# Performance work log

Measured on AMD Instinct MI355X. Metric: run time of the kernel, lower is better.

Reference implementation:

```python
import jax, jax.numpy as jnp
import numpy as np
from jax import lax

B, T, H = 4096, 2048, 32


def setup_inputs() -> dict:
    key = jax.random.key(0)
    ks = jax.random.split(key, 10)
    s = 1.0 / np.sqrt(H)  # PyTorch LSTM/Linear init scale
    x = jax.random.normal(ks[0], (B, T, 1), dtype=jnp.float32)
    lengths = jax.random.randint(ks[1], (B,), 1, T + 1, dtype=jnp.int32)
    u = lambda k, shape, sc: jax.random.uniform(k, shape, jnp.float32, -sc, sc)
    return {
        "x": x,
        "lengths": lengths,
        # backward-direction LSTM weights (only h_n[-1] is used by the head)
        "w_ih": u(ks[2], (4 * H, 1), s),
        "w_hh": u(ks[3], (4 * H, H), s),
        "b_ih": u(ks[4], (4 * H,), s),
        "b_hh": u(ks[5], (4 * H,), s),
        "fc_w": u(ks[6], (64, H), 1.0 / np.sqrt(H)),
        "fc_b": u(ks[7], (64,), 1.0 / np.sqrt(H)),
        "fc2_w": u(ks[8], (1, 64), 1.0 / np.sqrt(64)),
        "fc2_b": u(ks[9], (1,), 1.0 / np.sqrt(64)),
    }


def _backward_lstm_final(x, lengths, w_ih, w_hh, b_ih, b_hh):
    """Final hidden state of the backward direction of a packed BiLSTM.

    The backward direction reads each sequence from t=len-1 down to t=0 with
    zero initial state. Equivalently: scan padded x in reverse time order and
    only update (h, c) where t < length (packed-sequence semantics).
    """
    Bv, Tv, _ = x.shape
    ts = jnp.arange(Tv - 1, -1, -1)                       # reversed time indices
    xs_t = jnp.transpose(x[:, ::-1, :], (1, 0, 2))        # [T, B, 1]
    mask_t = ts[:, None] < lengths[None, :]               # [T, B]

    def step(carry, inp):
        h, c = carry
        xt, m = inp                                        # [B,1], [B]
        gates = xt @ w_ih.T + b_ih + h @ w_hh.T + b_hh     # [B, 4H]
        i, f, g, o = jnp.split(gates, 4, axis=-1)
        i = jax.nn.sigmoid(i)
        f = jax.nn.sigmoid(f)
        g = jnp.tanh(g)
        o = jax.nn.sigmoid(o)
        c_new = f * c + i * g
        h_new = o * jnp.tanh(c_new)
        mm = m[:, None]
        return (jnp.where(mm, h_new, h), jnp.where(mm, c_new, c)), None

    h0 = jnp.zeros((Bv, H), dtype=x.dtype)
    c0 = jnp.zeros((Bv, H), dtype=x.dtype)
    (h_n, _), _ = lax.scan(step, (h0, c0), (xs_t, mask_t))
    return h_n                                             # [B, H]


def reference(x, lengths, w_ih, w_hh, b_ih, b_hh, fc_w, fc_b, fc2_w, fc2_b):
    h_n = _backward_lstm_final(x, lengths, w_ih, w_hh, b_ih, b_hh)
    out = jax.nn.elu(h_n @ fc_w.T + fc_b)                  # [B, 64]
    out = jax.nn.sigmoid(out @ fc2_w.T + fc2_b)            # [B, 1]
    return out
```

## Files before the change

kernel.cpp:

```cpp
#include <hip/hip_runtime.h>
#include <hip/hip_bf16.h>

constexpr int BB = 4096;
constexpr int TT = 2048;
constexpr int HH = 32;

typedef float v2f __attribute__((ext_vector_type(2)));
typedef float v4f __attribute__((ext_vector_type(4)));
typedef _Float16 v2h __attribute__((ext_vector_type(2)));
typedef _Float16 v8h __attribute__((ext_vector_type(8)));

__device__ __forceinline__ float fexp2(float x) { return __builtin_amdgcn_exp2f(x); }
__device__ __forceinline__ float frcp(float x)  { return __builtin_amdgcn_rcpf(x); }
__device__ __forceinline__ float fsigmoid(float x) {
    return frcp(1.0f + fexp2(x * -1.4426950408889634f));
}
__device__ __forceinline__ float felu(float x) {
    return x > 0.0f ? x : (fexp2(x * 1.4426950408889634f) - 1.0f);
}

__global__ void sort_by_len_kernel(const int* __restrict__ lengths, int* __restrict__ perm) {
    __shared__ int hist[TT];
    __shared__ int csum[256];
    const int tid = threadIdx.x;
    for (int i = tid; i < TT; i += 256) hist[i] = 0;
    __syncthreads();
    for (int i = tid; i < BB; i += 256) atomicAdd(&hist[TT - lengths[i]], 1);
    __syncthreads();
    const int base = tid * 8;
    int loc[8];
    int s = 0;
#pragma unroll
    for (int j = 0; j < 8; ++j) { loc[j] = hist[base + j]; s += loc[j]; }
    csum[tid] = s;
    __syncthreads();
    for (int off = 1; off < 256; off <<= 1) {
        int v = (tid >= off) ? csum[tid - off] : 0;
        __syncthreads();
        csum[tid] += v;
        __syncthreads();
    }
    int run = csum[tid] - s;
#pragma unroll
    for (int j = 0; j < 8; ++j) { int t = loc[j]; hist[base + j] = run; run += t; }
    __syncthreads();
    for (int i = tid; i < BB; i += 256) {
        int pos = atomicAdd(&hist[TT - lengths[i]], 1);
        perm[pos] = i;
    }
}

__global__ __attribute__((amdgpu_flat_work_group_size(64, 64), amdgpu_waves_per_eu(1, 4)))
void lstm_kernel(const float* __restrict__ x, const int* __restrict__ lengths,
                 const float* __restrict__ w_ih, const float* __restrict__ w_hh,
                 const float* __restrict__ b_ih, const float* __restrict__ b_hh,
                 const float* __restrict__ fc_w, const float* __restrict__ fc_b,
                 const float* __restrict__ fc2_w, const float* __restrict__ fc2_b,
                 float* __restrict__ out, const int* __restrict__ perm) {
    __shared__ __align__(16) _Float16 hs[64];
    __shared__ float xbuf[64];

    const int lane = threadIdx.x;

    const int r0 = lane;
    const int r1 = lane + 64;

    const bool  lower  = lane < 32;
    const float NL2E   = -1.4426950408889634f;
    const float scale0 = NL2E;
    const float scale1 = lower ? 2.0f * NL2E : NL2E;
    const float amul   = lower ? 2.0f : 1.0f;
    const float badd   = lower ? -1.0f : 0.0f;

    v2h w0[16], w1[16];
    {
        const v2f* p0 = reinterpret_cast<const v2f*>(w_hh + r0 * 32);
        const v2f* p1 = reinterpret_cast<const v2f*>(w_hh + r1 * 32);
#pragma unroll
        for (int q = 0; q < 16; ++q) {
            v2f a = p0[q]; v2f bq = p1[q];
            w0[q] = (v2h){(_Float16)(a.x * scale0), (_Float16)(a.y * scale0)};
            w1[q] = (v2h){(_Float16)(bq.x * scale1), (_Float16)(bq.y * scale1)};
        }
    }
    const float wi0 = w_ih[r0] * scale0;
    const float wi1 = w_ih[r1] * scale1;
    const float bi0 = (b_ih[r0] + b_hh[r0]) * scale0;
    const float bi1 = (b_ih[r1] + b_hh[r1]) * scale1;

#pragma unroll
    for (int q = 0; q < 16; ++q) {
        asm volatile("" : "+v"(w0[q]), "+v"(w1[q]));
    }

    for (int phase = 0; phase < 2; ++phase) {
        const int k = phase ? (BB - 1 - (int)blockIdx.x) : (int)blockIdx.x;
        const int b = perm ? perm[k] : k;
        const int L = lengths[b];

        v8h hr[4];
#pragma unroll
        for (int q = 0; q < 4; ++q) hr[q] = (v8h)(_Float16)0.0f;
        float c = 0.0f;
        const float* xb = x + (size_t)b * TT;

        int t = L - 1;
        while (t >= 0) {
            const int tb = t & ~63;
            xbuf[lane] = xb[tb + lane];
            for (; t >= tb; --t) {
                const float xt = xbuf[t - tb];
                float a0  = fmaf(wi0, xt, bi0);
                float a1  = fmaf(wi1, xt, bi1);
                float a0b = 0.0f, a1b = 0.0f;
#pragma unroll
                for (int q = 0; q < 4; ++q) {
                    const v8h hh = hr[q];
                    const v2h p01 = __builtin_shufflevector(hh, hh, 0, 1);
                    const v2h p23 = __builtin_shufflevector(hh, hh, 2, 3);
                    const v2h p45 = __builtin_shufflevector(hh, hh, 4, 5);
                    const v2h p67 = __builtin_shufflevector(hh, hh, 6, 7);
                    a0  = __builtin_amdgcn_fdot2(w0[4*q+0], p01, a0,  false);
                    a0b = __builtin_amdgcn_fdot2(w0[4*q+1], p23, a0b, false);
                    a0  = __builtin_amdgcn_fdot2(w0[4*q+2], p45, a0,  false);
                    a0b = __builtin_amdgcn_fdot2(w0[4*q+3], p67, a0b, false);
                    a1  = __builtin_amdgcn_fdot2(w1[4*q+0], p01, a1,  false);
                    a1b = __builtin_amdgcn_fdot2(w1[4*q+1], p23, a1b, false);
                    a1  = __builtin_amdgcn_fdot2(w1[4*q+2], p45, a1,  false);
                    a1b = __builtin_amdgcn_fdot2(w1[4*q+3], p67, a1b, false);
                }
                const float g0 = a0 + a0b;
                const float g1 = a1 + a1b;
                const float s0 = frcp(1.0f + fexp2(g0));
                const float s1 = frcp(1.0f + fexp2(g1));
                const float v1 = fmaf(amul, s1, badd);
                const float ig = s0 * v1;
                const float igx = __shfl_xor(ig, 32);
                c = fmaf(s0, c, igx);
                const float tc = 1.0f - 2.0f * frcp(1.0f + fexp2(c * 2.8853900817779268f));
                const float hn = v1 * tc;
                hs[lane] = (_Float16)hn;
                const v8h* hp = reinterpret_cast<const v8h*>(hs + 32);
#pragma unroll
                for (int q = 0; q < 4; ++q) hr[q] = hp[q];
            }
        }

        float hf[32];
#pragma unroll
        for (int q = 0; q < 4; ++q) {
            const v8h hh = hr[q];
#pragma unroll
            for (int j = 0; j < 8; ++j) hf[8 * q + j] = (float)hh[j];
        }
        float a = fc_b[lane];
        {
            const v4f* fp = reinterpret_cast<const v4f*>(fc_w + lane * 32);
#pragma unroll
            for (int q = 0; q < 8; ++q) {
                const v4f f = fp[q];
                a = fmaf(f.x, hf[4 * q + 0], a);
                a = fmaf(f.y, hf[4 * q + 1], a);
                a = fmaf(f.z, hf[4 * q + 2], a);
                a = fmaf(f.w, hf[4 * q + 3], a);
            }
        }
        float partial = felu(a) * fc2_w[lane];
#pragma unroll
        for (int m = 32; m >= 1; m >>= 1) partial += __shfl_xor(partial, m, 64);
        if (lane == 0) out[b] = fsigmoid(partial + fc2_b[0]);
    }
}

extern "C" void kernel_launch(void* const* d_in, const int* in_sizes, int n_in,
                              void* d_out, int out_size, void* d_ws, size_t ws_size,
                              hipStream_t stream) {
    const float* x       = (const float*)d_in[0];
    const int*   lengths = (const int*)d_in[1];
    const float* w_ih    = (const float*)d_in[2];
    const float* w_hh    = (const float*)d_in[3];
    const float* b_ih    = (const float*)d_in[4];
    const float* b_hh    = (const float*)d_in[5];
    const float* fc_w    = (const float*)d_in[6];
    const float* fc_b    = (const float*)d_in[7];
    const float* fc2_w   = (const float*)d_in[8];
    const float* fc2_b   = (const float*)d_in[9];
    float* out = (float*)d_out;

    int* perm = nullptr;
    if (ws_size >= (size_t)BB * sizeof(int)) {
        perm = (int*)d_ws;
        hipLaunchKernelGGL(sort_by_len_kernel, dim3(1), dim3(256), 0, stream, lengths, perm);
    }
    hipLaunchKernelGGL(lstm_kernel, dim3(BB / 2), dim3(64), 0, stream,
                       x, lengths, w_ih, w_hh, b_ih, b_hh,
                       fc_w, fc_b, fc2_w, fc2_b, out, perm);
}
```

Before: 675.9 us.

## Broadcast hidden state via DPP and readlane instead of LDS round-trip

The per-step hidden-state exchange no longer goes through shared memory. Each lane packs its fp16 h with its neighbour's via a DPP quad swap, and 16 readlane ops broadcast the packed values from the upper half-wave into scalar registers. The x values come from a register via readlane instead of an LDS buffer, and the next 64-element chunk is prefetched one tile ahead. It also drops the waves_per_eu hint. This removes the LDS store/load latency on the serial recurrence, but adds 16 v_readlane instructions and their scalar dependency per step.

```diff
diff --git a/kernel.cpp b/kernel.cpp
--- a/kernel.cpp
+++ b/kernel.cpp
@@ -1,5 +1,4 @@
 #include <hip/hip_runtime.h>
-#include <hip/hip_bf16.h>
 
 constexpr int BB = 4096;
 constexpr int TT = 2048;
@@ -8,7 +7,6 @@
 typedef float v2f __attribute__((ext_vector_type(2)));
 typedef float v4f __attribute__((ext_vector_type(4)));
 typedef _Float16 v2h __attribute__((ext_vector_type(2)));
-typedef _Float16 v8h __attribute__((ext_vector_type(8)));
 
 __device__ __forceinline__ float fexp2(float x) { return __builtin_amdgcn_exp2f(x); }
 __device__ __forceinline__ float frcp(float x)  { return __builtin_amdgcn_rcpf(x); }
@@ -50,18 +48,14 @@
     }
 }
 
-__global__ __attribute__((amdgpu_flat_work_group_size(64, 64), amdgpu_waves_per_eu(1, 4)))
+__global__ __attribute__((amdgpu_flat_work_group_size(64, 64)))
 void lstm_kernel(const float* __restrict__ x, const int* __restrict__ lengths,
                  const float* __restrict__ w_ih, const float* __restrict__ w_hh,
                  const float* __restrict__ b_ih, const float* __restrict__ b_hh,
                  const float* __restrict__ fc_w, const float* __restrict__ fc_b,
                  const float* __restrict__ fc2_w, const float* __restrict__ fc2_b,
                  float* __restrict__ out, const int* __restrict__ perm) {
-    __shared__ __align__(16) _Float16 hs[64];
-    __shared__ float xbuf[64];
-
     const int lane = threadIdx.x;
-
     const int r0 = lane;
     const int r1 = lane + 64;
 
@@ -97,37 +91,35 @@
         const int k = phase ? (BB - 1 - (int)blockIdx.x) : (int)blockIdx.x;
         const int b = perm ? perm[k] : k;
         const int L = lengths[b];
-
-        v8h hr[4];
-#pragma unroll
-        for (int q = 0; q < 4; ++q) hr[q] = (v8h)(_Float16)0.0f;
-        float c = 0.0f;
         const float* xb = x + (size_t)b * TT;
 
+        int hp[16];
+#pragma unroll
+        for (int j = 0; j < 16; ++j) hp[j] = 0;
+        float c = 0.0f;
+
         int t = L - 1;
+        int tb = t & ~63;
+        float xv = xb[tb + lane];
         while (t >= 0) {
-            const int tb = t & ~63;
-            xbuf[lane] = xb[tb + lane];
+            const int tbn = tb - 64;
+            float xvn = 0.0f;
+            if (tbn >= 0) xvn = xb[tbn + lane];
+            const int xvi = __builtin_bit_cast(int, xv);
             for (; t >= tb; --t) {
-                const float xt = xbuf[t - tb];
+                const float xt = __builtin_bit_cast(float,
+                    __builtin_amdgcn_readlane(xvi, t - tb));
                 float a0  = fmaf(wi0, xt, bi0);
                 float a1  = fmaf(wi1, xt, bi1);
                 float a0b = 0.0f, a1b = 0.0f;
 #pragma unroll
-                for (int q = 0; q < 4; ++q) {
-                    const v8h hh = hr[q];
-                    const v2h p01 = __builtin_shufflevector(hh, hh, 0, 1);
-                    const v2h p23 = __builtin_shufflevector(hh, hh, 2, 3);
-                    const v2h p45 = __builtin_shufflevector(hh, hh, 4, 5);
-                    const v2h p67 = __builtin_shufflevector(hh, hh, 6, 7);
-                    a0  = __builtin_amdgcn_fdot2(w0[4*q+0], p01, a0,  false);
-                    a0b = __builtin_amdgcn_fdot2(w0[4*q+1], p23, a0b, false);
-                    a0  = __builtin_amdgcn_fdot2(w0[4*q+2], p45, a0,  false);
-                    a0b = __builtin_amdgcn_fdot2(w0[4*q+3], p67, a0b, false);
-                    a1  = __builtin_amdgcn_fdot2(w1[4*q+0], p01, a1,  false);
-                    a1b = __builtin_amdgcn_fdot2(w1[4*q+1], p23, a1b, false);
-                    a1  = __builtin_amdgcn_fdot2(w1[4*q+2], p45, a1,  false);
-                    a1b = __builtin_amdgcn_fdot2(w1[4*q+3], p67, a1b, false);
+                for (int q = 0; q < 16; q += 2) {
+                    const v2h pA = __builtin_bit_cast(v2h, hp[q]);
+                    const v2h pB = __builtin_bit_cast(v2h, hp[q + 1]);
+                    a0  = __builtin_amdgcn_fdot2(w0[q],     pA, a0,  false);
+                    a0b = __builtin_amdgcn_fdot2(w0[q + 1], pB, a0b, false);
+                    a1  = __builtin_amdgcn_fdot2(w1[q],     pA, a1,  false);
+                    a1b = __builtin_amdgcn_fdot2(w1[q + 1], pB, a1b, false);
                 }
                 const float g0 = a0 + a0b;
                 const float g1 = a1 + a1b;
@@ -139,19 +131,26 @@
                 c = fmaf(s0, c, igx);
                 const float tc = 1.0f - 2.0f * frcp(1.0f + fexp2(c * 2.8853900817779268f));
                 const float hn = v1 * tc;
-                hs[lane] = (_Float16)hn;
-                const v8h* hp = reinterpret_cast<const v8h*>(hs + 32);
+                const int hni = __builtin_bit_cast(int, hn);
+                const int hxi = __builtin_amdgcn_update_dpp(
+                    0, hni, 0xB1 , 0xF, 0xF, false);
+                const v2h pk = {(_Float16)hn,
+                                (_Float16)__builtin_bit_cast(float, hxi)};
+                const int pki = __builtin_bit_cast(int, pk);
 #pragma unroll
-                for (int q = 0; q < 4; ++q) hr[q] = hp[q];
+                for (int j = 0; j < 16; ++j)
+                    hp[j] = __builtin_amdgcn_readlane(pki, 32 + 2 * j);
             }
+            xv = xvn;
+            tb = tbn;
         }
 
         float hf[32];
 #pragma unroll
-        for (int q = 0; q < 4; ++q) {
-            const v8h hh = hr[q];
-#pragma unroll
-            for (int j = 0; j < 8; ++j) hf[8 * q + j] = (float)hh[j];
+        for (int j = 0; j < 16; ++j) {
+            const v2h p = __builtin_bit_cast(v2h, hp[j]);
+            hf[2 * j]     = (float)p[0];
+            hf[2 * j + 1] = (float)p[1];
         }
         float a = fc_b[lane];
         {
```

Measured after the change: 766.4 us. 13.4% more time.
